# Kernel tuning notes

Hardware: AMD Instinct MI355X
Metric: run time of the kernel (lower is better)

Reference implementation:

```python
import jax, jax.numpy as jnp
import numpy as np


def grid_sample_3d(vol, grid):
    """torch F.grid_sample 3D, mode='bilinear' (trilinear), align_corners=True.
    vol:  [B, C, Din, Hin, Win]
    grid: [B, Dout, Hout, Wout, 3] with xyz in [-1, 1] (x->W, y->H, z->D)
    returns [B, C, Dout, Hout, Wout]
    """
    B, C, Din, Hin, Win = vol.shape
    v = jnp.transpose(vol, (0, 2, 3, 4, 1))
    # align_corners=True: -1 -> 0, +1 -> size-1
    ix = (grid[..., 0] + 1.0) * 0.5 * (Win - 1)
    iy = (grid[..., 1] + 1.0) * 0.5 * (Hin - 1)
    iz = (grid[..., 2] + 1.0) * 0.5 * (Din - 1)
    x0 = jnp.floor(ix); y0 = jnp.floor(iy); z0 = jnp.floor(iz)
    wx = (ix - x0)[..., None]
    wy = (iy - y0)[..., None]
    wz = (iz - z0)[..., None]
    x0i = jnp.clip(x0.astype(jnp.int32), 0, Win - 1); x1i = jnp.clip(x0i + 1, 0, Win - 1)
    y0i = jnp.clip(y0.astype(jnp.int32), 0, Hin - 1); y1i = jnp.clip(y0i + 1, 0, Hin - 1)
    z0i = jnp.clip(z0.astype(jnp.int32), 0, Din - 1); z1i = jnp.clip(z0i + 1, 0, Din - 1)
    b = jnp.arange(B)[:, None, None, None]
    g = lambda z, y, x: v[b, z, y, x]  # [B, Dout, Hout, Wout, C]
    # interpolate along x, then y, then z
    c00 = g(z0i, y0i, x0i) * (1.0 - wx) + g(z0i, y0i, x1i) * wx
    c01 = g(z0i, y1i, x0i) * (1.0 - wx) + g(z0i, y1i, x1i) * wx
    c10 = g(z1i, y0i, x0i) * (1.0 - wx) + g(z1i, y0i, x1i) * wx
    c11 = g(z1i, y1i, x0i) * (1.0 - wx) + g(z1i, y1i, x1i) * wx
    c0 = c00 * (1.0 - wy) + c01 * wy
    c1 = c10 * (1.0 - wy) + c11 * wy
    out = c0 * (1.0 - wz) + c1 * wz  # [B, Dout, Hout, Wout, C]
    return jnp.transpose(out, (0, 4, 1, 2, 3))


def setup_inputs() -> dict:
    B, C, G, T = 2, 4, 128, 96
    key = jax.random.key(0)
    k1, k2, k3, k4 = jax.random.split(key, 4)
    grids = jax.random.uniform(k1, (B, G, G, G, 3), jnp.float32, minval=-1.0, maxval=1.0)
    deformation = jax.random.normal(k2, (B, 3, G, G, G), jnp.float32) * 0.1
    correction = jax.random.normal(k3, (B, C, G, G, G), jnp.float32) * 0.05
    template = jax.random.normal(k4, (B, C, T, T, T), jnp.float32)
    return {"grids": grids, "deformation": deformation, "correction": correction, "template": template}


def reference(grids, deformation, correction, template):
    # deformation: [B,3,W,H,D] -> [B,D,H,W,3]
    defp = jnp.transpose(deformation, (0, 4, 3, 2, 1))
    field = jnp.tanh(grids + defp)
    out = grid_sample_3d(template, field)           # [B,C,D,H,W]
    out = jnp.transpose(out, (0, 1, 4, 3, 2)) + correction  # [B,C,W,H,D]
    return (out, defp)
```

## Files before the change

kernel.cpp:

```cpp
#include <hip/hip_runtime.h>
#include <stdint.h>

#define G  128
#define TT 96
#define NB 2
#define NC 4
#define CS (TT * TT * TT)

typedef float f32x4 __attribute__((ext_vector_type(4)));
typedef float f32x2 __attribute__((ext_vector_type(2)));
typedef _Float16 f16x8 __attribute__((ext_vector_type(8)));
typedef _Float16 f16x8u __attribute__((ext_vector_type(8), aligned(8)));

__global__ __launch_bounds__(256) void tmpl_repack_f16(
        const float* __restrict__ tmpl, f16x8* __restrict__ out) {
    const int NP = NB * (CS / 2);
    int idx = blockIdx.x * 256 + threadIdx.x;
    if (idx >= NP) return;
    int b  = idx / (CS / 2);
    int s2 = idx - b * (CS / 2);
    const float* base = tmpl + (size_t)b * NC * CS + (size_t)s2 * 2;
    f16x8 o;
#pragma unroll
    for (int c = 0; c < NC; ++c) {
        f32x2 v = *(const f32x2*)(base + (size_t)c * CS);
        o[c]     = (_Float16)v.x;
        o[4 + c] = (_Float16)v.y;
    }
    out[idx] = o;
}

__global__ __launch_bounds__(256) void tmpl_repack_rec64(
        const float* __restrict__ tmpl, f16x8* __restrict__ out) {
    const int NV = NB * CS;
    int idx = blockIdx.x * 256 + threadIdx.x;
    if (idx >= NV) return;
    int b = idx / CS;
    int s = idx - b * CS;
    int x = s % TT;
    int t = s / TT;
    int y = t % TT;
    int z = t / TT;
    int x1 = min(x + 1, TT - 1);
    int y1 = min(y + 1, TT - 1);
    int z1 = min(z + 1, TT - 1);
    const float* tb = tmpl + (size_t)b * NC * CS;
    int zz[2] = {z, z1};
    int yy[2] = {y, y1};
    f16x8* dst = out + (size_t)idx * 4;
#pragma unroll
    for (int dz = 0; dz < 2; ++dz) {
#pragma unroll
        for (int dy = 0; dy < 2; ++dy) {
            size_t p0 = ((size_t)zz[dz] * TT + yy[dy]) * TT;
            f16x8 o;
#pragma unroll
            for (int c = 0; c < NC; ++c) {
                o[c]     = (_Float16)tb[(size_t)c * CS + p0 + x];
                o[4 + c] = (_Float16)tb[(size_t)c * CS + p0 + x1];
            }
            dst[dz * 2 + dy] = o;
        }
    }
}

template <int MODE>
__global__ __launch_bounds__(256, 4) void fused_sample_kernel(
        const float* __restrict__ grids,
        const float* __restrict__ deform,
        const float* __restrict__ corr,
        const f16x8* __restrict__ tmpl_pk,
        const float* __restrict__ tmpl_raw,
        float* __restrict__ out2,
        float* __restrict__ defp) {
    __shared__ float lds[3][32][36];

    int blk = blockIdx.x;
    int wt = blk & 3;
    int dt = (blk >> 2) & 3;
    int h  = (blk >> 4) & 127;
    int b  = blk >> 11;
    int w0 = wt << 5, d0 = dt << 5;
    int tid = threadIdx.x;

    for (int idx = tid; idx < 768; idx += 256) {
        int c   = idx >> 8;
        int rem = idx & 255;
        int i   = rem >> 3;
        int j4  = (rem & 7) << 2;
        size_t off = ((((size_t)b * 3 + c) * G + (w0 + i)) * G + h) * G + (d0 + j4);
        f32x4 v = __builtin_nontemporal_load((const f32x4*)(deform + off));
        *(f32x4*)&lds[c][i][j4] = v;
    }
    __syncthreads();

    for (int idx = tid; idx < 768; idx += 256) {
        int j = idx / 24;
        int t = idx - j * 24;
        size_t off = (((((size_t)b * G + (d0 + j)) * G + h) * G + w0) * 3) + (size_t)t * 4;
        f32x4 gv = __builtin_nontemporal_load((const f32x4*)(grids + off));
        float dv[4];
#pragma unroll
        for (int k = 0; k < 4; ++k) {
            int e = t * 4 + k;
            int i = e / 3;
            int c = e - 3 * i;
            float d = lds[c][i][j];
            dv[k] = d;
            lds[c][i][j] = tanhf(gv[k] + d);
        }
        __builtin_nontemporal_store(*(f32x4*)dv, (f32x4*)(defp + off));
    }
    __syncthreads();

    const float SC = 0.5f * (TT - 1);
    {
        int i  = tid >> 3;
        int j4 = (tid & 7) << 2;

        f32x4 fx = *(const f32x4*)&lds[0][i][j4];
        f32x4 fy = *(const f32x4*)&lds[1][i][j4];
        f32x4 fz = *(const f32x4*)&lds[2][i][j4];

        float wx[4], wy[4], wz[4];
        int base[4];
#pragma unroll
        for (int k = 0; k < 4; ++k) {
            float ix = (fx[k] + 1.0f) * SC;
            float iy = (fy[k] + 1.0f) * SC;
            float iz = (fz[k] + 1.0f) * SC;
            int x0 = min(max((int)floorf(ix), 0), TT - 2);
            int y0 = min(max((int)floorf(iy), 0), TT - 2);
            int z0 = min(max((int)floorf(iz), 0), TT - 2);
            wx[k] = ix - (float)x0;
            wy[k] = iy - (float)y0;
            wz[k] = iz - (float)z0;
            base[k] = (z0 * TT + y0) * TT + x0;
        }

        float r[4][4];
        if (MODE >= 1) {
            f16x8 v00[4], v01[4], v10[4], v11[4];
            if (MODE == 2) {
                const char* tb64 = (const char*)tmpl_pk + (size_t)b * ((size_t)CS * 64);
#pragma unroll
                for (int k = 0; k < 4; ++k) {
                    const f16x8* rec = (const f16x8*)(tb64 + (size_t)base[k] * 64);
                    v00[k] = rec[0];
                    v01[k] = rec[1];
                    v10[k] = rec[2];
                    v11[k] = rec[3];
                }
            } else {
                const char* tb16 = (const char*)tmpl_pk + (size_t)b * ((size_t)CS * 8);
#pragma unroll
                for (int k = 0; k < 4; ++k) {
                    v00[k] = *(const f16x8u*)(tb16 + ((size_t)base[k]) * 8);
                    v01[k] = *(const f16x8u*)(tb16 + ((size_t)(base[k] + TT)) * 8);
                    v10[k] = *(const f16x8u*)(tb16 + ((size_t)(base[k] + TT * TT)) * 8);
                    v11[k] = *(const f16x8u*)(tb16 + ((size_t)(base[k] + TT * TT + TT)) * 8);
                }
            }
#pragma unroll
            for (int k = 0; k < 4; ++k) {
                float mx = 1.0f - wx[k], my = 1.0f - wy[k], mz = 1.0f - wz[k];
                float a00 = my * mz, a01 = wy[k] * mz;
                float a10 = my * wz[k], a11 = wy[k] * wz[k];
#pragma unroll
                for (int c = 0; c < NC; ++c) {
                    float t00 = (float)v00[k][c] * mx + (float)v00[k][4 + c] * wx[k];
                    float t01 = (float)v01[k][c] * mx + (float)v01[k][4 + c] * wx[k];
                    float t10 = (float)v10[k][c] * mx + (float)v10[k][4 + c] * wx[k];
                    float t11 = (float)v11[k][c] * mx + (float)v11[k][4 + c] * wx[k];
                    r[k][c] = t00 * a00 + t01 * a01 + t10 * a10 + t11 * a11;
                }
            }
        } else {
#pragma unroll
            for (int k = 0; k < 4; ++k) {
                float mx = 1.0f - wx[k], my = 1.0f - wy[k], mz = 1.0f - wz[k];
                float w000 = mx * my * mz, w001 = wx[k] * my * mz;
                float w010 = mx * wy[k] * mz, w011 = wx[k] * wy[k] * mz;
                float w100 = mx * my * wz[k], w101 = wx[k] * my * wz[k];
                float w110 = mx * wy[k] * wz[k], w111 = wx[k] * wy[k] * wz[k];
                size_t i000 = (size_t)base[k];
                size_t i001 = i000 + 1;
                size_t i010 = i000 + TT;
                size_t i011 = i010 + 1;
                size_t i100 = i000 + TT * TT;
                size_t i101 = i100 + 1;
                size_t i110 = i100 + TT;
                size_t i111 = i110 + 1;
#pragma unroll
                for (int c = 0; c < NC; ++c) {
                    const float* tb = tmpl_raw + ((size_t)b * NC + c) * CS;
                    r[k][c] = tb[i000]*w000 + tb[i001]*w001 + tb[i010]*w010 + tb[i011]*w011
                            + tb[i100]*w100 + tb[i101]*w101 + tb[i110]*w110 + tb[i111]*w111;
                }
            }
        }

        int w = w0 + i, d = d0 + j4;
        size_t obase = ((((size_t)b * NC) * (size_t)G + w) * G + h) * G + d;
        const size_t cstride = (size_t)G * G * G;
#pragma unroll
        for (int c = 0; c < NC; ++c) {
            f32x4 cv = __builtin_nontemporal_load((const f32x4*)(corr + obase + c * cstride));
            f32x4 ov;
            ov.x = r[0][c] + cv.x;
            ov.y = r[1][c] + cv.y;
            ov.z = r[2][c] + cv.z;
            ov.w = r[3][c] + cv.w;
            __builtin_nontemporal_store(ov, (f32x4*)(out2 + obase + c * cstride));
        }
    }
}

extern "C" void kernel_launch(void* const* d_in, const int* in_sizes, int n_in,
                              void* d_out, int out_size, void* d_ws, size_t ws_size,
                              hipStream_t stream) {
    const float* grids  = (const float*)d_in[0];
    const float* deform = (const float*)d_in[1];
    const float* corr   = (const float*)d_in[2];
    const float* tmpl   = (const float*)d_in[3];
    float* out2 = (float*)d_out;
    float* defp = out2 + (size_t)NB * NC * G * G * G;
    f16x8* tmpl_pk = (f16x8*)d_ws;

    const size_t ws2 = (size_t)NB * CS * 64;
    const size_t ws1 = (size_t)NB * CS * 8;

    int nblk = NB * G * 16;

    if (ws_size >= ws2) {
        int nv = NB * CS;
        tmpl_repack_rec64<<<(nv + 255) / 256, 256, 0, stream>>>(tmpl, tmpl_pk);
        fused_sample_kernel<2><<<nblk, 256, 0, stream>>>(
            grids, deform, corr, tmpl_pk, tmpl, out2, defp);
    } else if (ws_size >= ws1) {
        int np = NB * (CS / 2);
        tmpl_repack_f16<<<(np + 255) / 256, 256, 0, stream>>>(tmpl, tmpl_pk);
        fused_sample_kernel<1><<<nblk, 256, 0, stream>>>(
            grids, deform, corr, tmpl_pk, tmpl, out2, defp);
    } else {
        fused_sample_kernel<0><<<nblk, 256, 0, stream>>>(
            grids, deform, corr, tmpl_pk, tmpl, out2, defp);
    }
}
```

Baseline: 359.6 us.

## Repack template as 16-byte x-pair records instead of 64-byte corner records

Replaces the 64-byte per-voxel record holding all eight corners with a 16-byte record per voxel holding that voxel and its x+1 neighbour for all four channels in fp16. The sampler now gathers four aligned 16-byte loads per sample at offsets 0, TT, TT*TT and TT*TT+TT. This cuts the repack workspace writes and the gather footprint by a factor of four, which should help cache hit rates, at the cost of four scattered loads per sample instead of one contiguous 64-byte record. It also drops the occupancy hint from the launch bounds, which may change register allocation.

Result: slower. 376.9 us (+4.8%).

```diff
diff --git a/kernel.cpp b/kernel.cpp
--- a/kernel.cpp
+++ b/kernel.cpp
@@ -30,7 +30,7 @@
     out[idx] = o;
 }
 
-__global__ __launch_bounds__(256) void tmpl_repack_rec64(
+__global__ __launch_bounds__(256) void tmpl_repack_dual16(
         const float* __restrict__ tmpl, f16x8* __restrict__ out) {
     const int NV = NB * CS;
     int idx = blockIdx.x * 256 + threadIdx.x;
@@ -38,34 +38,21 @@
     int b = idx / CS;
     int s = idx - b * CS;
     int x = s % TT;
-    int t = s / TT;
-    int y = t % TT;
-    int z = t / TT;
     int x1 = min(x + 1, TT - 1);
-    int y1 = min(y + 1, TT - 1);
-    int z1 = min(z + 1, TT - 1);
+    int rowbase = s - x;
     const float* tb = tmpl + (size_t)b * NC * CS;
-    int zz[2] = {z, z1};
-    int yy[2] = {y, y1};
-    f16x8* dst = out + (size_t)idx * 4;
-#pragma unroll
-    for (int dz = 0; dz < 2; ++dz) {
-#pragma unroll
-        for (int dy = 0; dy < 2; ++dy) {
-            size_t p0 = ((size_t)zz[dz] * TT + yy[dy]) * TT;
-            f16x8 o;
-#pragma unroll
-            for (int c = 0; c < NC; ++c) {
-                o[c]     = (_Float16)tb[(size_t)c * CS + p0 + x];
-                o[4 + c] = (_Float16)tb[(size_t)c * CS + p0 + x1];
-            }
-            dst[dz * 2 + dy] = o;
-        }
-    }
+    f16x8 o;
+#pragma unroll
+    for (int c = 0; c < NC; ++c) {
+        const float* row = tb + (size_t)c * CS + rowbase;
+        o[c]     = (_Float16)row[x];
+        o[4 + c] = (_Float16)row[x1];
+    }
+    out[idx] = o;
 }
 
 template <int MODE>
-__global__ __launch_bounds__(256, 4) void fused_sample_kernel(
+__global__ __launch_bounds__(256) void fused_sample_kernel(
         const float* __restrict__ grids,
         const float* __restrict__ deform,
         const float* __restrict__ corr,
@@ -141,15 +128,14 @@
         float r[4][4];
         if (MODE >= 1) {
             f16x8 v00[4], v01[4], v10[4], v11[4];
-            if (MODE == 2) {
-                const char* tb64 = (const char*)tmpl_pk + (size_t)b * ((size_t)CS * 64);
+            if (MODE == 3) {
+                const f16x8* tb = tmpl_pk + (size_t)b * CS;
 #pragma unroll
                 for (int k = 0; k < 4; ++k) {
-                    const f16x8* rec = (const f16x8*)(tb64 + (size_t)base[k] * 64);
-                    v00[k] = rec[0];
-                    v01[k] = rec[1];
-                    v10[k] = rec[2];
-                    v11[k] = rec[3];
+                    v00[k] = tb[base[k]];
+                    v01[k] = tb[base[k] + TT];
+                    v10[k] = tb[base[k] + TT * TT];
+                    v11[k] = tb[base[k] + TT * TT + TT];
                 }
             } else {
                 const char* tb16 = (const char*)tmpl_pk + (size_t)b * ((size_t)CS * 8);
@@ -227,15 +213,15 @@
     float* defp = out2 + (size_t)NB * NC * G * G * G;
     f16x8* tmpl_pk = (f16x8*)d_ws;
 
-    const size_t ws2 = (size_t)NB * CS * 64;
+    const size_t ws3 = (size_t)NB * CS * 16;
     const size_t ws1 = (size_t)NB * CS * 8;
 
     int nblk = NB * G * 16;
 
-    if (ws_size >= ws2) {
+    if (ws_size >= ws3) {
         int nv = NB * CS;
-        tmpl_repack_rec64<<<(nv + 255) / 256, 256, 0, stream>>>(tmpl, tmpl_pk);
-        fused_sample_kernel<2><<<nblk, 256, 0, stream>>>(
+        tmpl_repack_dual16<<<(nv + 255) / 256, 256, 0, stream>>>(tmpl, tmpl_pk);
+        fused_sample_kernel<3><<<nblk, 256, 0, stream>>>(
             grids, deform, corr, tmpl_pk, tmpl, out2, defp);
     } else if (ws_size >= ws1) {
         int np = NB * (CS / 2);
```
